# Kernel tuning notes

Hardware: AMD Instinct MI355X
Metric: run time of the kernel (lower is better)

## Reference

```python
import jax, jax.numpy as jnp
import numpy as np

C_IN, C_OUT, K = 2048, 1024, 2  # k=2 -> 5x5 correlation window
B, H, W = 4, 64, 64


def conv1x1(x, w, b):
    # x: [B,C,H,W], w: [O,C], b: [O]
    return jnp.einsum('bchw,oc->bohw', x, w) + b[None, :, None, None]


def bn_star(x, Kstd=3.0):
    # torch.std is unbiased (ddof=1); clip outliers above mu+K*std to 1
    mu = jnp.mean(x, axis=0, keepdims=True)
    std = jnp.std(x, axis=0, ddof=1, keepdims=True)
    lim = mu + Kstd * std
    return jnp.where(x > lim, jnp.float32(1.0), x)


def match_trans(curr_F, prev_F, prev_M):
    # curr_F/prev_F: [B,2048,H,W]; prev_M: [B,1024,H,W]
    b, c, h, w = prev_F.shape
    prev_nc = jnp.sum(prev_F, axis=1)  # [B,H,W]
    curr_nc = jnp.sum(curr_F, axis=1)  # [B,H,W]
    pad_nc = jnp.pad(prev_nc, ((0, 0), (K, K), (K, K)))
    pad_M = jnp.pad(prev_M, ((0, 0), (0, 0), (K, K), (K, K)))
    # shifted copies: shift(i,j)(y,x) = prev_nc_padded(y-i, x-j)
    shifts = jnp.stack([pad_nc[:, K - i:K - i + h, K - j:K - j + w]
                        for i in range(-K, K + 1) for j in range(-K, K + 1)], axis=0)  # [25,B,H,W]
    # sum_filter(prev_F) summed over channels == C * 5x5 local sum of prev_nc
    denom = curr_nc * (jnp.float32(c) * jnp.sum(shifts, axis=0))  # [B,H,W]
    aligned = jnp.zeros_like(prev_M)
    idx = 0
    for i in range(-K, K + 1):
        for j in range(-K, K + 1):
            mask_ij = curr_nc * shifts[idx] / denom  # [B,H,W]
            aligned = aligned + mask_ij[:, None] * pad_M[:, :, K - i:K - i + h, K - j:K - j + w]
            idx += 1
    return aligned


def setup_inputs() -> dict:
    key = jax.random.key(0)
    ks = jax.random.split(key, 16)
    s = jnp.float32(0.02)
    inp = {
        'curr_F': jax.random.uniform(ks[0], (B, C_IN, H, W), jnp.float32),
        'prev_F': jax.random.uniform(ks[1], (B, C_IN, H, W), jnp.float32),
        'prev_M': jax.random.normal(ks[2], (B, C_OUT, H, W), jnp.float32),
        'Wz_w': jax.random.normal(ks[3], (C_OUT, C_IN), jnp.float32) * s,
        'Wz_b': jnp.zeros((C_OUT,), jnp.float32),
        'Wr_w': jax.random.normal(ks[4], (C_OUT, C_IN), jnp.float32) * s,
        'Wr_b': jnp.zeros((C_OUT,), jnp.float32),
        'W_w': jax.random.normal(ks[5], (C_OUT, C_IN), jnp.float32) * s,
        'W_b': jnp.zeros((C_OUT,), jnp.float32),
        'Uz_w': jax.random.normal(ks[6], (C_OUT, C_OUT), jnp.float32) * s,
        'Uz_b': jnp.zeros((C_OUT,), jnp.float32),
        'Ur_w': jax.random.normal(ks[7], (C_OUT, C_OUT), jnp.float32) * s,
        'Ur_b': jnp.zeros((C_OUT,), jnp.float32),
        'U_w': jax.random.normal(ks[8], (C_OUT, C_OUT), jnp.float32) * s,
        'U_b': jnp.zeros((C_OUT,), jnp.float32),
        'body': 1,
    }
    return inp


def reference(curr_F, prev_F, prev_M, Wz_w, Wz_b, Wr_w, Wr_b, W_w, W_b,
              Uz_w, Uz_b, Ur_w, Ur_b, U_w, U_b, body):
    if body:
        aligned = match_trans(curr_F, prev_F, prev_M)
    else:
        aligned = prev_M
    zt = bn_star(jax.nn.relu(conv1x1(curr_F, Wz_w, Wz_b) + conv1x1(aligned, Uz_w, Uz_b)))
    rt = bn_star(jax.nn.relu(conv1x1(curr_F, Wr_w, Wr_b) + conv1x1(aligned, Ur_w, Ur_b)))
    M = jax.nn.relu(conv1x1(curr_F, W_w, W_b) + conv1x1(aligned * rt, U_w, U_b))
    curr_M = (1.0 - zt) * aligned + zt * M
    return curr_M
```

## Files before the change

kernel.cpp:

```cpp
#include <hip/hip_runtime.h>
#include <hip/hip_bf16.h>

namespace {

constexpr int NB = 4;
constexpr int CI = 2048;
constexpr int CO = 1024;
constexpr int HW = 4096;
constexpr int MTOT = NB * HW;

typedef __attribute__((ext_vector_type(8))) short bf16x8;
typedef __attribute__((ext_vector_type(4))) float f32x4;
typedef __hip_bfloat16 bf16;

__device__ __forceinline__ void g2l16(void* lds, const void* g) {
  __builtin_amdgcn_global_load_lds((const __attribute__((address_space(1))) void*)g,
                                   (__attribute__((address_space(3))) void*)lds,
                                   16, 0, 0);
}

__global__ void zero_k(float* __restrict__ p, int n) {
  int i = blockIdx.x * 256 + threadIdx.x;
  if (i < n) p[i] = 0.f;
}

__global__ void castw6_k(const float* s0, const float* s1, const float* s2,
                         const float* s3, const float* s4, const float* s5,
                         bf16* d0, bf16* d1, bf16* d2, bf16* d3, bf16* d4, bf16* d5) {
  int y = blockIdx.y;
  const float* s = (y == 0) ? s0 : (y == 1) ? s1 : (y == 2) ? s2 : (y == 3) ? s3 : (y == 4) ? s4 : s5;
  bf16* d = (y == 0) ? d0 : (y == 1) ? d1 : (y == 2) ? d2 : (y == 3) ? d3 : (y == 4) ? d4 : d5;
  int n4 = ((y < 3) ? CI * CO : CO * CO) >> 2;
  int i = blockIdx.x * 256 + threadIdx.x;
  if (i < n4) {
    float4 v = ((const float4*)s)[i];
    union { ushort4 u; bf16 h[4]; } pk;
    pk.h[0] = __float2bfloat16(v.x);
    pk.h[1] = __float2bfloat16(v.y);
    pk.h[2] = __float2bfloat16(v.z);
    pk.h[3] = __float2bfloat16(v.w);
    ((ushort4*)d)[i] = pk.u;
  }
}

__global__ void nc_sum_k(const float* __restrict__ src, float* __restrict__ dst) {
  int p = blockIdx.x * 256 + threadIdx.x;
  int c0 = blockIdx.y * 128;
  int b = blockIdx.z;
  const float* s = src + ((long)b * CI + c0) * HW + p;
  float a = 0.f;
  #pragma unroll 8
  for (int c = 0; c < 128; ++c) a += s[(long)c * HW];
  atomicAdd(dst + b * HW + p, a);
}

template <typename T> __device__ __forceinline__ T cvt_out(float v);
template <> __device__ __forceinline__ float cvt_out<float>(float v) { return v; }
template <> __device__ __forceinline__ bf16 cvt_out<bf16>(float v) { return __float2bfloat16(v); }

template <typename TO>
__global__ void transpose_k(const float* __restrict__ src, TO* __restrict__ dst, int R, int S) {
  __shared__ float tile[32][33];
  int b = blockIdx.z;
  int r0 = blockIdx.x * 32, s0 = blockIdx.y * 32;
  int ts = threadIdx.x & 31, tr = threadIdx.x >> 5;
  const float* sp = src + ((long)b * R + r0) * S + s0;
  #pragma unroll
  for (int i = 0; i < 32; i += 8) tile[tr + i][ts] = sp[(long)(tr + i) * S + ts];
  __syncthreads();
  TO* dp = dst + ((long)b * S + s0) * R + r0;
  #pragma unroll
  for (int i = 0; i < 32; i += 8) dp[(long)(tr + i) * R + ts] = cvt_out<TO>(tile[ts][tr + i]);
}

__global__ void boxinv_k(const float* __restrict__ nc, float* __restrict__ invden) {
  int i = blockIdx.x * 256 + threadIdx.x;
  int b = i >> 12, p = i & 4095;
  int y = p >> 6, x = p & 63;
  float s = 0.f;
  #pragma unroll
  for (int dy = -2; dy <= 2; ++dy) {
    int yy = y + dy;
    if ((unsigned)yy >= 64u) continue;
    #pragma unroll
    for (int dx = -2; dx <= 2; ++dx) {
      int xx = x + dx;
      if ((unsigned)xx >= 64u) continue;
      s += nc[b * HW + yy * 64 + xx];
    }
  }
  invden[i] = 1.f / (2048.f * s);
}

__global__ void align_k(const float* __restrict__ pmcl, const float* __restrict__ nc,
                        const float* __restrict__ invden, const int* __restrict__ body,
                        float* __restrict__ af, bf16* __restrict__ ah) {
  int bp = blockIdx.x;
  int b = bp >> 12, p = bp & 4095;
  int y = p >> 6, x = p & 63;
  int c = threadIdx.x * 4;
  float4 acc = make_float4(0.f, 0.f, 0.f, 0.f);
  if (body[0]) {
    #pragma unroll
    for (int dy = -2; dy <= 2; ++dy) {
      int yy = y + dy;
      if ((unsigned)yy >= 64u) continue;
      #pragma unroll
      for (int dx = -2; dx <= 2; ++dx) {
        int xx = x + dx;
        if ((unsigned)xx >= 64u) continue;
        int sp = yy * 64 + xx;
        float w = nc[b * HW + sp];
        float4 v = *(const float4*)(pmcl + ((long)b * HW + sp) * CO + c);
        acc.x += w * v.x; acc.y += w * v.y; acc.z += w * v.z; acc.w += w * v.w;
      }
    }
    float s = invden[bp];
    acc.x *= s; acc.y *= s; acc.z *= s; acc.w *= s;
  } else {
    acc = *(const float4*)(pmcl + (long)bp * CO + c);
  }
  long o = (long)bp * CO + c;
  *(float4*)(af + o) = acc;
  union { ushort4 u; bf16 h[4]; } pk;
  pk.h[0] = __float2bfloat16(acc.x);
  pk.h[1] = __float2bfloat16(acc.y);
  pk.h[2] = __float2bfloat16(acc.z);
  pk.h[3] = __float2bfloat16(acc.w);
  *(ushort4*)(ah + o) = pk.u;
}

template <int MODE>
__global__ __launch_bounds__(512, 2) void gemm256(
    const bf16* __restrict__ A1, const bf16* __restrict__ B1,
    const bf16* __restrict__ A2, const bf16* __restrict__ B2,
    const float* __restrict__ bias1, const float* __restrict__ bias2,
    const float* __restrict__ ztp, const float* __restrict__ alig,
    const bf16* __restrict__ aligh,
    float* __restrict__ outf, bf16* __restrict__ outh) {
  constexpr int ldA1 = CI, ldB1 = CI, ldA2 = CO, ldB2 = CO;
  constexpr int NT1 = CI / 32;
  constexpr int NT = NT1 + CO / 32;
  __shared__ __align__(16) char lds[131072];
  const int t = threadIdx.x, lane = t & 63, wid = t >> 6;
  const int wm = wid >> 2, wn = wid & 3;
  const int m0 = blockIdx.x * 256, n0 = blockIdx.y * 256;
  const int fr = lane & 15, kq = lane >> 4;

  const int b0i = (wid << 7) + lane;
  const int line0 = b0i >> 3;
  const int c3 = (b0i & 7) ^ (line0 & 7);
  const int row0 = 2 * line0 + (c3 >> 2);
  const int k16 = c3 & 3;
  const char* pa1 = (const char*)A1 + (((size_t)(m0 + row0) * ldA1 + k16 * 8) << 1);
  const char* pa1h = pa1 + ((size_t)ldA1 << 5);
  const char* pb1 = (const char*)B1 + (((size_t)(n0 + row0) * ldB1 + k16 * 8) << 1);
  const char* pb1h = pb1 + ((size_t)ldB1 << 5);
  const char* pa2 = (const char*)A2 + (((size_t)(m0 + row0) * ldA2 + k16 * 8) << 1);
  const char* pa2h = pa2 + ((size_t)ldA2 << 5);
  const char* pb2 = (const char*)B2 + (((size_t)(n0 + row0) * ldB2 + k16 * 8) << 1);
  const char* pb2h = pb2 + ((size_t)ldB2 << 5);

  auto STAGE = [&](int s) {
    const char *sa, *sah, *sb, *sbh;
    if (s < NT1) {
      size_t so = (size_t)s << 6;
      sa = pa1 + so; sah = pa1h + so; sb = pb1 + so; sbh = pb1h + so;
    } else {
      size_t so = (size_t)(s - NT1) << 6;
      sa = pa2 + so; sah = pa2h + so; sb = pb2 + so; sbh = pb2h + so;
    }
    char* d = lds + ((s & 3) << 15) + (wid << 11) + (lane << 4);
    g2l16(d, sa);
    g2l16(d + 1024, sah);
    g2l16(d + 16384, sb);
    g2l16(d + 17408, sbh);
  };

  int offA[8], offB[4];
  #pragma unroll
  for (int mi = 0; mi < 8; ++mi) {
    int r = (wm << 7) + (mi << 4) + fr;
    int ln = r >> 1;
    int cc = ((r & 1) << 2) | kq;
    offA[mi] = (ln << 7) + ((cc ^ (ln & 7)) << 4);
  }
  #pragma unroll
  for (int ni = 0; ni < 4; ++ni) {
    int r = (wn << 6) + (ni << 4) + fr;
    int ln = r >> 1;
    int cc = ((r & 1) << 2) | kq;
    offB[ni] = 16384 + (ln << 7) + ((cc ^ (ln & 7)) << 4);
  }

  f32x4 acc[8][4] = {};
  bf16x8 avA[8], avB[8], bv[4];

  STAGE(0); STAGE(1); STAGE(2);
  asm volatile("s_waitcnt vmcnt(8)" ::: "memory");
  __builtin_amdgcn_s_barrier();
  asm volatile("" ::: "memory");
  #pragma unroll
  for (int mi = 0; mi < 8; ++mi) avA[mi] = *(const bf16x8*)(lds + offA[mi]);

#define PHASE(p, AVC, AVN, W, DOSTAGE, READNEXT)                                   \
  {                                                                                \
    const char* bufp_ = lds + (((p) & 3) << 15);                                   \
    _Pragma("unroll")                                                              \
    for (int ni_ = 0; ni_ < 4; ++ni_) bv[ni_] = *(const bf16x8*)(bufp_ + offB[ni_]);\
    if (DOSTAGE) STAGE((p) + 3);                                                   \
    asm volatile("s_waitcnt vmcnt(" #W ")" ::: "memory");                          \
    __builtin_amdgcn_s_barrier();                                                  \
    asm volatile("" ::: "memory");                                                 \
    __builtin_amdgcn_s_setprio(1);                                                 \
    _Pragma("unroll")                                                              \
    for (int mi_ = 0; mi_ < 8; ++mi_)                                              \
      _Pragma("unroll")                                                            \
      for (int ni_ = 0; ni_ < 4; ++ni_)                                            \
        acc[mi_][ni_] =                                                            \
            __builtin_amdgcn_mfma_f32_16x16x32_bf16(AVC[mi_], bv[ni_], acc[mi_][ni_], 0, 0, 0); \
    __builtin_amdgcn_s_setprio(0);                                                 \
    if (READNEXT) {                                                                \
      const char* bufn_ = lds + ((((p) + 1) & 3) << 15);                           \
      _Pragma("unroll")                                                            \
      for (int mi_ = 0; mi_ < 8; ++mi_) AVN[mi_] = *(const bf16x8*)(bufn_ + offA[mi_]); \
    }                                                                              \
    asm volatile("" ::: "memory");                                                 \
    __builtin_amdgcn_s_barrier();                                                  \
  }

  #pragma unroll 1
  for (int p = 0; p < NT - 4; p += 2) {
    PHASE(p, avA, avB, 8, 1, 1);
    PHASE(p + 1, avB, avA, 8, 1, 1);
  }
  PHASE(NT - 4, avA, avB, 8, 1, 1);
  PHASE(NT - 3, avB, avA, 4, 0, 1);
  PHASE(NT - 2, avA, avB, 0, 0, 1);
  PHASE(NT - 1, avB, avA, 0, 0, 0);
#undef PHASE

  #pragma unroll
  for (int mi = 0; mi < 8; ++mi) {
    const int r0 = m0 + (wm << 7) + (mi << 4) + (kq << 2);
    #pragma unroll
    for (int ni = 0; ni < 4; ++ni) {
      const int col = n0 + (wn << 6) + (ni << 4) + fr;
      const float bsum = bias1[col] + bias2[col];
      #pragma unroll
      for (int j = 0; j < 4; ++j) {
        const size_t idx = (size_t)(r0 + j) * CO + col;
        float v = acc[mi][ni][j] + bsum;
        if (MODE == 0) {
          outf[idx] = fmaxf(v, 0.f);
        } else if (MODE == 3) {
          float rt = fmaxf(v, 0.f);
          outh[idx] = __float2bfloat16(__bfloat162float(aligh[idx]) * rt);
        } else {
          float m = fmaxf(v, 0.f);
          float z = ztp[idx];
          outf[idx] = (1.f - z) * alig[idx] + z * m;
        }
      }
    }
  }
}

}

extern "C" void kernel_launch(void* const* d_in, const int* in_sizes, int n_in,
                              void* d_out, int out_size, void* d_ws, size_t ws_size,
                              hipStream_t stream) {
  const float* curr_F = (const float*)d_in[0];
  const float* prev_F = (const float*)d_in[1];
  const float* prev_M = (const float*)d_in[2];
  const float* Wz_w = (const float*)d_in[3];
  const float* Wz_b = (const float*)d_in[4];
  const float* Wr_w = (const float*)d_in[5];
  const float* Wr_b = (const float*)d_in[6];
  const float* W_w  = (const float*)d_in[7];
  const float* W_b  = (const float*)d_in[8];
  const float* Uz_w = (const float*)d_in[9];
  const float* Uz_b = (const float*)d_in[10];
  const float* Ur_w = (const float*)d_in[11];
  const float* Ur_b = (const float*)d_in[12];
  const float* U_w  = (const float*)d_in[13];
  const float* U_b  = (const float*)d_in[14];
  const int* body   = (const int*)d_in[15];
  float* out = (float*)d_out;

  char* ws = (char*)d_ws;
  const size_t M64 = 1ull << 26;
  const size_t M32 = 1ull << 25;
  bf16*  currF_h   = (bf16*)(ws);
  float* prevM_cl  = (float*)(ws + M64);
  float* zt        = (float*)(ws + M64);
  float* align_f   = (float*)(ws + 2 * M64);
  bf16*  align_h   = (bf16*)(ws + 3 * M64);
  float* currM_cl  = (float*)(ws + 3 * M64 + M32);
  bf16*  ar_h      = (bf16*)(ws + 4 * M64 + M32);
  char*  wb        = ws + 4 * M64 + 2 * M32;
  bf16* Wz_h = (bf16*)wb;
  bf16* Wr_h = Wz_h + (size_t)CO * CI;
  bf16* W_h  = Wr_h + (size_t)CO * CI;
  bf16* Uz_h = W_h  + (size_t)CO * CI;
  bf16* Ur_h = Uz_h + (size_t)CO * CO;
  bf16* U_h  = Ur_h + (size_t)CO * CO;
  float* prev_nc = (float*)(U_h + (size_t)CO * CO);
  float* invden  = prev_nc + NB * HW;

  castw6_k<<<dim3((CI * CO) / 1024, 6), 256, 0, stream>>>(
      Wz_w, Wr_w, W_w, Uz_w, Ur_w, U_w, Wz_h, Wr_h, W_h, Uz_h, Ur_h, U_h);

  zero_k<<<dim3((NB * HW) / 256), 256, 0, stream>>>(prev_nc, NB * HW);
  nc_sum_k<<<dim3(HW / 256, CI / 128, NB), 256, 0, stream>>>(prev_F, prev_nc);

  transpose_k<bf16><<<dim3(CI / 32, HW / 32, NB), 256, 0, stream>>>(curr_F, currF_h, CI, HW);
  transpose_k<float><<<dim3(CO / 32, HW / 32, NB), 256, 0, stream>>>(prev_M, prevM_cl, CO, HW);

  boxinv_k<<<dim3((NB * HW) / 256), 256, 0, stream>>>(prev_nc, invden);
  align_k<<<dim3(NB * HW), 256, 0, stream>>>(prevM_cl, prev_nc, invden, body, align_f, align_h);

  dim3 gg(MTOT / 256, CO / 256);
  gemm256<0><<<gg, 512, 0, stream>>>(currF_h, Wz_h, align_h, Uz_h,
                                     Wz_b, Uz_b, nullptr, nullptr, nullptr, zt, nullptr);
  gemm256<3><<<gg, 512, 0, stream>>>(currF_h, Wr_h, align_h, Ur_h,
                                     Wr_b, Ur_b, nullptr, nullptr, align_h, nullptr, ar_h);
  gemm256<2><<<gg, 512, 0, stream>>>(currF_h, W_h, ar_h, U_h,
                                     W_b, U_b, zt, align_f, nullptr, currM_cl, nullptr);

  transpose_k<float><<<dim3(HW / 32, CO / 32, NB), 256, 0, stream>>>(currM_cl, out, HW, CO);
}
```

Measured before the change: 591.1 us.

## Restructure GEMM main loop into 8-phase K=64 pipeline with double buffering

```diff
diff --git a/kernel.cpp b/kernel.cpp
--- a/kernel.cpp
+++ b/kernel.cpp
@@ -131,121 +131,119 @@
 }
 
 template <int MODE>
-__global__ __launch_bounds__(512, 2) void gemm256(
+__global__ __launch_bounds__(512, 2) void gemm8p(
     const bf16* __restrict__ A1, const bf16* __restrict__ B1,
     const bf16* __restrict__ A2, const bf16* __restrict__ B2,
     const float* __restrict__ bias1, const float* __restrict__ bias2,
     const float* __restrict__ ztp, const float* __restrict__ alig,
     const bf16* __restrict__ aligh,
     float* __restrict__ outf, bf16* __restrict__ outh) {
-  constexpr int ldA1 = CI, ldB1 = CI, ldA2 = CO, ldB2 = CO;
-  constexpr int NT1 = CI / 32;
-  constexpr int NT = NT1 + CO / 32;
+  constexpr int NT1 = CI / 64;
+  constexpr int NT = NT1 + CO / 64;
   __shared__ __align__(16) char lds[131072];
   const int t = threadIdx.x, lane = t & 63, wid = t >> 6;
   const int wm = wid >> 2, wn = wid & 3;
   const int m0 = blockIdx.x * 256, n0 = blockIdx.y * 256;
   const int fr = lane & 15, kq = lane >> 4;
 
-  const int b0i = (wid << 7) + lane;
-  const int line0 = b0i >> 3;
-  const int c3 = (b0i & 7) ^ (line0 & 7);
-  const int row0 = 2 * line0 + (c3 >> 2);
-  const int k16 = c3 & 3;
-  const char* pa1 = (const char*)A1 + (((size_t)(m0 + row0) * ldA1 + k16 * 8) << 1);
-  const char* pa1h = pa1 + ((size_t)ldA1 << 5);
-  const char* pb1 = (const char*)B1 + (((size_t)(n0 + row0) * ldB1 + k16 * 8) << 1);
-  const char* pb1h = pb1 + ((size_t)ldB1 << 5);
-  const char* pa2 = (const char*)A2 + (((size_t)(m0 + row0) * ldA2 + k16 * 8) << 1);
-  const char* pa2h = pa2 + ((size_t)ldA2 << 5);
-  const char* pb2 = (const char*)B2 + (((size_t)(n0 + row0) * ldB2 + k16 * 8) << 1);
-  const char* pb2h = pb2 + ((size_t)ldB2 << 5);
-
-  auto STAGE = [&](int s) {
-    const char *sa, *sah, *sb, *sbh;
+  const int cc0 = (t & 7) ^ ((t >> 3) & 7);
+  const int row_l = ((t >> 3) << 1) + (cc0 >> 2);
+  const int k16 = cc0 & 3;
+  const char* pa1 = (const char*)A1 + (((size_t)(m0 + row_l) * CI + k16 * 8) << 1);
+  const char* pb1 = (const char*)B1 + (((size_t)(n0 + row_l) * CI + k16 * 8) << 1);
+  const char* pa2 = (const char*)A2 + (((size_t)(m0 + row_l) * CO + k16 * 8) << 1);
+  const char* pb2 = (const char*)B2 + (((size_t)(n0 + row_l) * CO + k16 * 8) << 1);
+
+  auto ST = [&](int s, int isB, int rh, int kh) {
+    const char* g;
     if (s < NT1) {
-      size_t so = (size_t)s << 6;
-      sa = pa1 + so; sah = pa1h + so; sb = pb1 + so; sbh = pb1h + so;
+      g = (isB ? pb1 : pa1) + ((size_t)s << 7) + (kh << 6) + (rh ? 524288 : 0);
     } else {
-      size_t so = (size_t)(s - NT1) << 6;
-      sa = pa2 + so; sah = pa2h + so; sb = pb2 + so; sbh = pb2h + so;
+      g = (isB ? pb2 : pa2) + ((size_t)(s - NT1) << 7) + (kh << 6) + (rh ? 262144 : 0);
     }
-    char* d = lds + ((s & 3) << 15) + (wid << 11) + (lane << 4);
-    g2l16(d, sa);
-    g2l16(d + 1024, sah);
-    g2l16(d + 16384, sb);
-    g2l16(d + 17408, sbh);
+    g2l16(lds + ((s & 1) << 16) + (isB << 15) + (kh << 14) + (rh << 13) + (t << 4), g);
   };
 
   int offA[8], offB[4];
   #pragma unroll
-  for (int mi = 0; mi < 8; ++mi) {
-    int r = (wm << 7) + (mi << 4) + fr;
+  for (int m = 0; m < 8; ++m) {
+    int r = wm * 16 + m * 32 + fr;
     int ln = r >> 1;
-    int cc = ((r & 1) << 2) | kq;
-    offA[mi] = (ln << 7) + ((cc ^ (ln & 7)) << 4);
-  }
-  #pragma unroll
-  for (int ni = 0; ni < 4; ++ni) {
-    int r = (wn << 6) + (ni << 4) + fr;
+    int c = ((r & 1) << 2) | kq;
+    offA[m] = (ln << 7) + ((c ^ (ln & 7)) << 4);
+  }
+  #pragma unroll
+  for (int n = 0; n < 4; ++n) {
+    int r = wn * 16 + n * 64 + fr;
     int ln = r >> 1;
-    int cc = ((r & 1) << 2) | kq;
-    offB[ni] = 16384 + (ln << 7) + ((cc ^ (ln & 7)) << 4);
+    int c = ((r & 1) << 2) | kq;
+    offB[n] = 32768 + (ln << 7) + ((c ^ (ln & 7)) << 4);
   }
 
   f32x4 acc[8][4] = {};
-  bf16x8 avA[8], avB[8], bv[4];
-
-  STAGE(0); STAGE(1); STAGE(2);
-  asm volatile("s_waitcnt vmcnt(8)" ::: "memory");
+  bf16x8 av[4], bv[4];
+
+  ST(0, 0, 0, 0); ST(0, 1, 0, 0); ST(0, 1, 1, 0); ST(0, 0, 1, 0);
+  ST(0, 0, 0, 1); ST(0, 1, 0, 1); ST(0, 1, 1, 1); ST(0, 0, 1, 1);
+  ST(1, 0, 0, 0); ST(1, 1, 0, 0); ST(1, 1, 1, 0); ST(1, 0, 1, 0);
+  asm volatile("s_waitcnt vmcnt(4)" ::: "memory");
   __builtin_amdgcn_s_barrier();
   asm volatile("" ::: "memory");
-  #pragma unroll
-  for (int mi = 0; mi < 8; ++mi) avA[mi] = *(const bf16x8*)(lds + offA[mi]);
-
-#define PHASE(p, AVC, AVN, W, DOSTAGE, READNEXT)                                   \
-  {                                                                                \
-    const char* bufp_ = lds + (((p) & 3) << 15);                                   \
-    _Pragma("unroll")                                                              \
-    for (int ni_ = 0; ni_ < 4; ++ni_) bv[ni_] = *(const bf16x8*)(bufp_ + offB[ni_]);\
-    if (DOSTAGE) STAGE((p) + 3);                                                   \
-    asm volatile("s_waitcnt vmcnt(" #W ")" ::: "memory");                          \
-    __builtin_amdgcn_s_barrier();                                                  \
-    asm volatile("" ::: "memory");                                                 \
-    __builtin_amdgcn_s_setprio(1);                                                 \
-    _Pragma("unroll")                                                              \
-    for (int mi_ = 0; mi_ < 8; ++mi_)                                              \
-      _Pragma("unroll")                                                            \
-      for (int ni_ = 0; ni_ < 4; ++ni_)                                            \
-        acc[mi_][ni_] =                                                            \
-            __builtin_amdgcn_mfma_f32_16x16x32_bf16(AVC[mi_], bv[ni_], acc[mi_][ni_], 0, 0, 0); \
-    __builtin_amdgcn_s_setprio(0);                                                 \
-    if (READNEXT) {                                                                \
-      const char* bufn_ = lds + ((((p) + 1) & 3) << 15);                           \
-      _Pragma("unroll")                                                            \
-      for (int mi_ = 0; mi_ < 8; ++mi_) AVN[mi_] = *(const bf16x8*)(bufn_ + offA[mi_]); \
-    }                                                                              \
-    asm volatile("" ::: "memory");                                                 \
-    __builtin_amdgcn_s_barrier();                                                  \
-  }
+
+#define BAR do { asm volatile("" ::: "memory"); __builtin_amdgcn_s_barrier(); \
+                 asm volatile("" ::: "memory"); } while (0)
+#define MFMA16(ACM)                                                           \
+  __builtin_amdgcn_s_setprio(1);                                              \
+  _Pragma("unroll") for (int mi_ = 0; mi_ < 4; ++mi_)                         \
+  _Pragma("unroll") for (int ni_ = 0; ni_ < 4; ++ni_)                         \
+    acc[(ACM) + mi_][ni_] = __builtin_amdgcn_mfma_f32_16x16x32_bf16(          \
+        av[mi_], bv[ni_], acc[(ACM) + mi_][ni_], 0, 0, 0);                    \
+  __builtin_amdgcn_s_setprio(0);
 
   #pragma unroll 1
-  for (int p = 0; p < NT - 4; p += 2) {
-    PHASE(p, avA, avB, 8, 1, 1);
-    PHASE(p + 1, avB, avA, 8, 1, 1);
-  }
-  PHASE(NT - 4, avA, avB, 8, 1, 1);
-  PHASE(NT - 3, avB, avA, 4, 0, 1);
-  PHASE(NT - 2, avA, avB, 0, 0, 1);
-  PHASE(NT - 1, avB, avA, 0, 0, 0);
-#undef PHASE
+  for (int s = 0; s < NT; ++s) {
+    const char* buf = lds + ((s & 1) << 16);
+    const bool st1 = (s + 1 < NT), st2 = (s + 2 < NT);
+    #pragma unroll
+    for (int i = 0; i < 4; ++i) av[i] = *(const bf16x8*)(buf + offA[i]);
+    #pragma unroll
+    for (int i = 0; i < 4; ++i) bv[i] = *(const bf16x8*)(buf + offB[i]);
+    if (st1) { ST(s + 1, 0, 0, 1); ST(s + 1, 1, 0, 1); }
+    BAR;
+    MFMA16(0);
+    BAR;
+    #pragma unroll
+    for (int i = 0; i < 4; ++i) av[i] = *(const bf16x8*)(buf + offA[4 + i]);
+    if (st1) { ST(s + 1, 1, 1, 1); ST(s + 1, 0, 1, 1); }
+    BAR;
+    MFMA16(4);
+    BAR;
+    #pragma unroll
+    for (int i = 0; i < 4; ++i) av[i] = *(const bf16x8*)(buf + 16384 + offA[i]);
+    #pragma unroll
+    for (int i = 0; i < 4; ++i) bv[i] = *(const bf16x8*)(buf + 16384 + offB[i]);
+    if (st2) { ST(s + 2, 0, 0, 0); ST(s + 2, 1, 0, 0); }
+    BAR;
+    MFMA16(0);
+    BAR;
+    #pragma unroll
+    for (int i = 0; i < 4; ++i) av[i] = *(const bf16x8*)(buf + 16384 + offA[4 + i]);
+    if (st2) { ST(s + 2, 1, 1, 0); ST(s + 2, 0, 1, 0); }
+    BAR;
+    MFMA16(4);
+    if (s < NT - 2) asm volatile("s_waitcnt vmcnt(4)" ::: "memory");
+    else            asm volatile("s_waitcnt vmcnt(0)" ::: "memory");
+    BAR;
+  }
+#undef MFMA16
+#undef BAR
 
   #pragma unroll
   for (int mi = 0; mi < 8; ++mi) {
-    const int r0 = m0 + (wm << 7) + (mi << 4) + (kq << 2);
+    const int r0 = m0 + wm * 16 + mi * 32 + kq * 4;
     #pragma unroll
     for (int ni = 0; ni < 4; ++ni) {
-      const int col = n0 + (wn << 6) + (ni << 4) + fr;
+      const int col = n0 + wn * 16 + ni * 64 + fr;
       const float bsum = bias1[col] + bias2[col];
       #pragma unroll
       for (int j = 0; j < 4; ++j) {
@@ -322,12 +320,12 @@
   align_k<<<dim3(NB * HW), 256, 0, stream>>>(prevM_cl, prev_nc, invden, body, align_f, align_h);
 
   dim3 gg(MTOT / 256, CO / 256);
-  gemm256<0><<<gg, 512, 0, stream>>>(currF_h, Wz_h, align_h, Uz_h,
-                                     Wz_b, Uz_b, nullptr, nullptr, nullptr, zt, nullptr);
-  gemm256<3><<<gg, 512, 0, stream>>>(currF_h, Wr_h, align_h, Ur_h,
-                                     Wr_b, Ur_b, nullptr, nullptr, align_h, nullptr, ar_h);
-  gemm256<2><<<gg, 512, 0, stream>>>(currF_h, W_h, ar_h, U_h,
-                                     W_b, U_b, zt, align_f, nullptr, currM_cl, nullptr);
+  gemm8p<0><<<gg, 512, 0, stream>>>(currF_h, Wz_h, align_h, Uz_h,
+                                    Wz_b, Uz_b, nullptr, nullptr, nullptr, zt, nullptr);
+  gemm8p<3><<<gg, 512, 0, stream>>>(currF_h, Wr_h, align_h, Ur_h,
+                                    Wr_b, Ur_b, nullptr, nullptr, align_h, nullptr, ar_h);
+  gemm8p<2><<<gg, 512, 0, stream>>>(currF_h, W_h, ar_h, U_h,
+                                    W_b, U_b, zt, align_f, nullptr, currM_cl, nullptr);
 
   transpose_k<float><<<dim3(HW / 32, CO / 32, NB), 256, 0, stream>>>(currM_cl, out, HW, CO);
 }
```

Result: slower. 607.6 us (+2.8%).

## Fuse output transpose into final GEMM epilogue and drop fp32 aligned buffer

Applied to the files above, without the earlier changes.

```diff
diff --git a/kernel.cpp b/kernel.cpp
--- a/kernel.cpp
+++ b/kernel.cpp
@@ -94,7 +94,7 @@
 
 __global__ void align_k(const float* __restrict__ pmcl, const float* __restrict__ nc,
                         const float* __restrict__ invden, const int* __restrict__ body,
-                        float* __restrict__ af, bf16* __restrict__ ah) {
+                        bf16* __restrict__ ah) {
   int bp = blockIdx.x;
   int b = bp >> 12, p = bp & 4095;
   int y = p >> 6, x = p & 63;
@@ -120,14 +120,12 @@
   } else {
     acc = *(const float4*)(pmcl + (long)bp * CO + c);
   }
-  long o = (long)bp * CO + c;
-  *(float4*)(af + o) = acc;
   union { ushort4 u; bf16 h[4]; } pk;
   pk.h[0] = __float2bfloat16(acc.x);
   pk.h[1] = __float2bfloat16(acc.y);
   pk.h[2] = __float2bfloat16(acc.z);
   pk.h[3] = __float2bfloat16(acc.w);
-  *(ushort4*)(ah + o) = pk.u;
+  *(ushort4*)(ah + (long)bp * CO + c) = pk.u;
 }
 
 template <int MODE>
@@ -135,10 +133,9 @@
     const bf16* __restrict__ A1, const bf16* __restrict__ B1,
     const bf16* __restrict__ A2, const bf16* __restrict__ B2,
     const float* __restrict__ bias1, const float* __restrict__ bias2,
-    const float* __restrict__ ztp, const float* __restrict__ alig,
-    const bf16* __restrict__ aligh,
-    float* __restrict__ outf, bf16* __restrict__ outh) {
-  constexpr int ldA1 = CI, ldB1 = CI, ldA2 = CO, ldB2 = CO;
+    const float* __restrict__ ztp, const bf16* __restrict__ aligh,
+    float* __restrict__ outf, bf16* __restrict__ outh,
+    float* __restrict__ outcf) {
   constexpr int NT1 = CI / 32;
   constexpr int NT = NT1 + CO / 32;
   __shared__ __align__(16) char lds[131072];
@@ -152,14 +149,14 @@
   const int c3 = (b0i & 7) ^ (line0 & 7);
   const int row0 = 2 * line0 + (c3 >> 2);
   const int k16 = c3 & 3;
-  const char* pa1 = (const char*)A1 + (((size_t)(m0 + row0) * ldA1 + k16 * 8) << 1);
-  const char* pa1h = pa1 + ((size_t)ldA1 << 5);
-  const char* pb1 = (const char*)B1 + (((size_t)(n0 + row0) * ldB1 + k16 * 8) << 1);
-  const char* pb1h = pb1 + ((size_t)ldB1 << 5);
-  const char* pa2 = (const char*)A2 + (((size_t)(m0 + row0) * ldA2 + k16 * 8) << 1);
-  const char* pa2h = pa2 + ((size_t)ldA2 << 5);
-  const char* pb2 = (const char*)B2 + (((size_t)(n0 + row0) * ldB2 + k16 * 8) << 1);
-  const char* pb2h = pb2 + ((size_t)ldB2 << 5);
+  const char* pa1 = (const char*)A1 + (((size_t)(m0 + row0) * CI + k16 * 8) << 1);
+  const char* pa1h = pa1 + ((size_t)CI << 5);
+  const char* pb1 = (const char*)B1 + (((size_t)(n0 + row0) * CI + k16 * 8) << 1);
+  const char* pb1h = pb1 + ((size_t)CI << 5);
+  const char* pa2 = (const char*)A2 + (((size_t)(m0 + row0) * CO + k16 * 8) << 1);
+  const char* pa2h = pa2 + ((size_t)CO << 5);
+  const char* pb2 = (const char*)B2 + (((size_t)(n0 + row0) * CO + k16 * 8) << 1);
+  const char* pb2h = pb2 + ((size_t)CO << 5);
 
   auto STAGE = [&](int s) {
     const char *sa, *sah, *sb, *sbh;
@@ -194,51 +191,39 @@
   }
 
   f32x4 acc[8][4] = {};
-  bf16x8 avA[8], avB[8], bv[4];
 
   STAGE(0); STAGE(1); STAGE(2);
-  asm volatile("s_waitcnt vmcnt(8)" ::: "memory");
-  __builtin_amdgcn_s_barrier();
-  asm volatile("" ::: "memory");
-  #pragma unroll
-  for (int mi = 0; mi < 8; ++mi) avA[mi] = *(const bf16x8*)(lds + offA[mi]);
-
-#define PHASE(p, AVC, AVN, W, DOSTAGE, READNEXT)                                   \
-  {                                                                                \
-    const char* bufp_ = lds + (((p) & 3) << 15);                                   \
-    _Pragma("unroll")                                                              \
-    for (int ni_ = 0; ni_ < 4; ++ni_) bv[ni_] = *(const bf16x8*)(bufp_ + offB[ni_]);\
-    if (DOSTAGE) STAGE((p) + 3);                                                   \
-    asm volatile("s_waitcnt vmcnt(" #W ")" ::: "memory");                          \
-    __builtin_amdgcn_s_barrier();                                                  \
-    asm volatile("" ::: "memory");                                                 \
-    __builtin_amdgcn_s_setprio(1);                                                 \
-    _Pragma("unroll")                                                              \
-    for (int mi_ = 0; mi_ < 8; ++mi_)                                              \
-      _Pragma("unroll")                                                            \
-      for (int ni_ = 0; ni_ < 4; ++ni_)                                            \
-        acc[mi_][ni_] =                                                            \
-            __builtin_amdgcn_mfma_f32_16x16x32_bf16(AVC[mi_], bv[ni_], acc[mi_][ni_], 0, 0, 0); \
-    __builtin_amdgcn_s_setprio(0);                                                 \
-    if (READNEXT) {                                                                \
-      const char* bufn_ = lds + ((((p) + 1) & 3) << 15);                           \
-      _Pragma("unroll")                                                            \
-      for (int mi_ = 0; mi_ < 8; ++mi_) AVN[mi_] = *(const bf16x8*)(bufn_ + offA[mi_]); \
-    }                                                                              \
-    asm volatile("" ::: "memory");                                                 \
-    __builtin_amdgcn_s_barrier();                                                  \
-  }
+
+  auto PHASE = [&](int tp, int W, bool dostage) {
+    if (dostage) STAGE(tp + 3);
+    if (W == 12)      asm volatile("s_waitcnt vmcnt(12)" ::: "memory");
+    else if (W == 8)  asm volatile("s_waitcnt vmcnt(8)" ::: "memory");
+    else if (W == 4)  asm volatile("s_waitcnt vmcnt(4)" ::: "memory");
+    else              asm volatile("s_waitcnt vmcnt(0)" ::: "memory");
+    __builtin_amdgcn_s_barrier();
+    asm volatile("" ::: "memory");
+    const char* buf = lds + ((tp & 3) << 15);
+    bf16x8 av[8], bv[4];
+    #pragma unroll
+    for (int mi = 0; mi < 8; ++mi) av[mi] = *(const bf16x8*)(buf + offA[mi]);
+    #pragma unroll
+    for (int ni = 0; ni < 4; ++ni) bv[ni] = *(const bf16x8*)(buf + offB[ni]);
+    __builtin_amdgcn_s_setprio(1);
+    #pragma unroll
+    for (int mi = 0; mi < 8; ++mi)
+      #pragma unroll
+      for (int ni = 0; ni < 4; ++ni)
+        acc[mi][ni] = __builtin_amdgcn_mfma_f32_16x16x32_bf16(av[mi], bv[ni], acc[mi][ni], 0, 0, 0);
+    __builtin_amdgcn_s_setprio(0);
+    asm volatile("" ::: "memory");
+    __builtin_amdgcn_s_barrier();
+  };
 
   #pragma unroll 1
-  for (int p = 0; p < NT - 4; p += 2) {
-    PHASE(p, avA, avB, 8, 1, 1);
-    PHASE(p + 1, avB, avA, 8, 1, 1);
-  }
-  PHASE(NT - 4, avA, avB, 8, 1, 1);
-  PHASE(NT - 3, avB, avA, 4, 0, 1);
-  PHASE(NT - 2, avA, avB, 0, 0, 1);
-  PHASE(NT - 1, avB, avA, 0, 0, 0);
-#undef PHASE
+  for (int tt = 0; tt < NT - 3; ++tt) PHASE(tt, 12, true);
+  PHASE(NT - 3, 8, false);
+  PHASE(NT - 2, 4, false);
+  PHASE(NT - 1, 0, false);
 
   #pragma unroll
   for (int mi = 0; mi < 8; ++mi) {
@@ -247,19 +232,30 @@
     for (int ni = 0; ni < 4; ++ni) {
       const int col = n0 + (wn << 6) + (ni << 4) + fr;
       const float bsum = bias1[col] + bias2[col];
-      #pragma unroll
-      for (int j = 0; j < 4; ++j) {
-        const size_t idx = (size_t)(r0 + j) * CO + col;
-        float v = acc[mi][ni][j] + bsum;
-        if (MODE == 0) {
-          outf[idx] = fmaxf(v, 0.f);
-        } else if (MODE == 3) {
-          float rt = fmaxf(v, 0.f);
-          outh[idx] = __float2bfloat16(__bfloat162float(aligh[idx]) * rt);
-        } else {
-          float m = fmaxf(v, 0.f);
+      if (MODE == 2) {
+        const int bb = r0 >> 12, p0 = r0 & 4095;
+        float4 o;
+        float* po = &o.x;
+        #pragma unroll
+        for (int j = 0; j < 4; ++j) {
+          const size_t idx = (size_t)(r0 + j) * CO + col;
+          float m = fmaxf(acc[mi][ni][j] + bsum, 0.f);
           float z = ztp[idx];
-          outf[idx] = (1.f - z) * alig[idx] + z * m;
+          float a = __bfloat162float(aligh[idx]);
+          po[j] = (1.f - z) * a + z * m;
+        }
+        *(float4*)(outcf + ((size_t)bb * CO + col) * HW + p0) = o;
+      } else {
+        #pragma unroll
+        for (int j = 0; j < 4; ++j) {
+          const size_t idx = (size_t)(r0 + j) * CO + col;
+          float v = acc[mi][ni][j] + bsum;
+          if (MODE == 0) {
+            outf[idx] = fmaxf(v, 0.f);
+          } else {
+            float rt = fmaxf(v, 0.f);
+            outh[idx] = __float2bfloat16(__bfloat162float(aligh[idx]) * rt);
+          }
         }
       }
     }
@@ -295,11 +291,9 @@
   bf16*  currF_h   = (bf16*)(ws);
   float* prevM_cl  = (float*)(ws + M64);
   float* zt        = (float*)(ws + M64);
-  float* align_f   = (float*)(ws + 2 * M64);
-  bf16*  align_h   = (bf16*)(ws + 3 * M64);
-  float* currM_cl  = (float*)(ws + 3 * M64 + M32);
-  bf16*  ar_h      = (bf16*)(ws + 4 * M64 + M32);
-  char*  wb        = ws + 4 * M64 + 2 * M32;
+  bf16*  align_h   = (bf16*)(ws + 2 * M64);
+  bf16*  ar_h      = (bf16*)(ws + 2 * M64 + M32);
+  char*  wb        = ws + 2 * M64 + 2 * M32;
   bf16* Wz_h = (bf16*)wb;
   bf16* Wr_h = Wz_h + (size_t)CO * CI;
   bf16* W_h  = Wr_h + (size_t)CO * CI;
@@ -319,15 +313,13 @@
   transpose_k<float><<<dim3(CO / 32, HW / 32, NB), 256, 0, stream>>>(prev_M, prevM_cl, CO, HW);
 
   boxinv_k<<<dim3((NB * HW) / 256), 256, 0, stream>>>(prev_nc, invden);
-  align_k<<<dim3(NB * HW), 256, 0, stream>>>(prevM_cl, prev_nc, invden, body, align_f, align_h);
+  align_k<<<dim3(NB * HW), 256, 0, stream>>>(prevM_cl, prev_nc, invden, body, align_h);
 
   dim3 gg(MTOT / 256, CO / 256);
   gemm256<0><<<gg, 512, 0, stream>>>(currF_h, Wz_h, align_h, Uz_h,
-                                     Wz_b, Uz_b, nullptr, nullptr, nullptr, zt, nullptr);
+                                     Wz_b, Uz_b, nullptr, nullptr, zt, nullptr, nullptr);
   gemm256<3><<<gg, 512, 0, stream>>>(currF_h, Wr_h, align_h, Ur_h,
-                                     Wr_b, Ur_b, nullptr, nullptr, align_h, nullptr, ar_h);
+                                     Wr_b, Ur_b, nullptr, align_h, nullptr, ar_h, nullptr);
   gemm256<2><<<gg, 512, 0, stream>>>(currF_h, W_h, ar_h, U_h,
-                                     W_b, U_b, zt, align_f, nullptr, currM_cl, nullptr);
-
-  transpose_k<float><<<dim3(HW / 32, CO / 32, NB), 256, 0, stream>>>(currM_cl, out, HW, CO);
-}
+                                     W_b, U_b, zt, align_h, nullptr, nullptr, out);
+}
```

Measured after the change: 554.5 us. -6.2%, faster.
